# Kernel optimization log

Hardware: AMD Instinct MI355X
Metric: run time of the kernel (lower is better)

Reference implementation:

```python
import jax, jax.numpy as jnp
import numpy as np
from jax import lax

EPS = 1e-6

def setup_inputs() -> dict:
    key = jax.random.key(0)
    ks = jax.random.split(key, 5)
    B, C, H, W = 32, 128, 128, 128
    D = 128
    bcff = jax.random.normal(ks[0], (B, C, H, W), dtype=jnp.float32)
    cur_active = jax.random.randint(ks[1], (B, 1, H, W), 0, 2) > 0
    gamma = jnp.ones((C,), dtype=jnp.float32)
    beta = jnp.zeros((C,), dtype=jnp.float32)
    # trunc_normal_(std=0.02) approximated by clipped normal
    mask_token = jnp.clip(0.02 * jax.random.normal(ks[2], (1, C, 1, 1), dtype=jnp.float32), -0.02, 0.02)
    fan_in = C * 1 * 1
    bound = 1.0 / np.sqrt(fan_in)
    conv_w = jax.random.uniform(ks[3], (D, C, 1, 1), dtype=jnp.float32, minval=-bound, maxval=bound)
    conv_b = jnp.zeros((D,), dtype=jnp.float32)
    return {"bcff": bcff, "cur_active": cur_active, "gamma": gamma, "beta": beta,
            "mask_token": mask_token, "conv_w": conv_w, "conv_b": conv_b}

def reference(bcff, cur_active, gamma, beta, mask_token, conv_w, conv_b):
    # Sparse channels-first LayerNorm: normalize over C at every position; positions
    # that are inactive are overwritten by mask_token (torch zero-fills then where-selects,
    # so the math is identical).
    mu = jnp.mean(bcff, axis=1, keepdims=True)                      # (B,1,H,W)
    var = jnp.mean(jnp.square(bcff - mu), axis=1, keepdims=True)    # biased var, as F.layer_norm
    normed = (bcff - mu) * lax.rsqrt(var + EPS)
    normed = normed * gamma[None, :, None, None] + beta[None, :, None, None]
    # mask-token fill
    filled = jnp.where(cur_active, normed, mask_token)              # (B,C,H,W)
    # 1x1 conv projection (SAME padding, stride 1)
    out = lax.conv_general_dilated(filled, conv_w, window_strides=(1, 1), padding='SAME',
                                   dimension_numbers=('NCHW', 'OIHW', 'NCHW'))
    return out + conv_b[None, :, None, None]
```

## Files before the change

### kernel.cpp

```cpp
#include <hip/hip_runtime.h>


#define CC   128
#define DD   128
#define HWW  16384
#define PP   128
#define NTHREADS 512

typedef __attribute__((ext_vector_type(8))) short short8;
typedef __attribute__((ext_vector_type(4))) float f32x4;

__device__ __forceinline__ float b2f(unsigned short u) {
    return __uint_as_float(((unsigned int)u) << 16);
}
__device__ __forceinline__ unsigned short f2b(float f) {
    unsigned int u = __float_as_uint(f);
    return (unsigned short)((u + 0x7FFFu + ((u >> 16) & 1u)) >> 16);
}
__device__ __forceinline__ unsigned int pk2(float lo, float hi) {
    return (unsigned int)f2b(lo) | ((unsigned int)f2b(hi) << 16);
}
__device__ __forceinline__ float ldf(const void* p, int i, bool bf) {
    return bf ? b2f(((const unsigned short*)p)[i]) : ((const float*)p)[i];
}

__global__ void prep_pack_w(const void* __restrict__ w, unsigned short* __restrict__ wpack,
                            const void* __restrict__ gamma) {
    const bool bf = (((const unsigned int*)gamma)[0] == 0x3F803F80u);
    int e = blockIdx.x * blockDim.x + threadIdx.x;
    int j = e & 7, lane = (e >> 3) & 63, kk = (e >> 9) & 3, wv = e >> 11;
    int d = wv * 16 + (lane & 15);
    int c = kk * 32 + ((lane >> 4) & 3) * 8 + j;
    wpack[e] = f2b(ldf(w, d * CC + c, bf));
}

__global__ __launch_bounds__(NTHREADS, 4)
void spark_densify_mfma(const void* __restrict__ x,
                        const void* __restrict__ act,
                        const void* __restrict__ gam,
                        const void* __restrict__ bet,
                        const void* __restrict__ mtok,
                        const unsigned short* __restrict__ wpack,
                        const void* __restrict__ bias,
                        float* __restrict__ out)
{
    __shared__ __align__(16) uint4 afrag[8 * 4 * 64];
    __shared__ float ps_s[8][PP];
    __shared__ float ps_q[8][PP];
    __shared__ float st_mu[PP];
    __shared__ float st_rs[PP];

    const int t    = threadIdx.x;
    const int bk   = blockIdx.x;
    const int b    = bk >> 7;
    const int pos0 = (bk & 127) * PP;

    const bool bf = (((const unsigned int*)gam)[0] == 0x3F803F80u);
    bool mint = true;
    #pragma unroll
    for (int i = 0; i < 16; ++i) mint = mint && (((const unsigned int*)act)[i] <= 1u);

    const int pq = t & 31;
    const int cg = t >> 5;
    const long xbase = (long)b * CC * HWW + pos0 + pq * 4;

    float4 v[8];
    float s0=0.f,s1=0.f,s2=0.f,s3=0.f;
    float q0=0.f,q1=0.f,q2=0.f,q3=0.f;
    if (!bf) {
        const float* xf = (const float*)x;
        #pragma unroll
        for (int i = 0; i < 8; ++i) {
            v[i] = *(const float4*)(xf + xbase + (long)(cg * 8 + i) * HWW);
            s0 += v[i].x; q0 = fmaf(v[i].x, v[i].x, q0);
            s1 += v[i].y; q1 = fmaf(v[i].y, v[i].y, q1);
            s2 += v[i].z; q2 = fmaf(v[i].z, v[i].z, q2);
            s3 += v[i].w; q3 = fmaf(v[i].w, v[i].w, q3);
        }
    } else {
        const unsigned short* xh = (const unsigned short*)x;
        #pragma unroll
        for (int i = 0; i < 8; ++i) {
            const ushort4 u = *(const ushort4*)(xh + xbase + (long)(cg * 8 + i) * HWW);
            v[i] = make_float4(b2f(u.x), b2f(u.y), b2f(u.z), b2f(u.w));
            s0 += v[i].x; q0 = fmaf(v[i].x, v[i].x, q0);
            s1 += v[i].y; q1 = fmaf(v[i].y, v[i].y, q1);
            s2 += v[i].z; q2 = fmaf(v[i].z, v[i].z, q2);
            s3 += v[i].w; q3 = fmaf(v[i].w, v[i].w, q3);
        }
    }
    s0 += __shfl_xor(s0, 32); q0 += __shfl_xor(q0, 32);
    s1 += __shfl_xor(s1, 32); q1 += __shfl_xor(q1, 32);
    s2 += __shfl_xor(s2, 32); q2 += __shfl_xor(q2, 32);
    s3 += __shfl_xor(s3, 32); q3 += __shfl_xor(q3, 32);

    const int wv_  = t >> 6;
    const int lane = t & 63;
    if (lane < 32) {
        *(float4*)&ps_s[wv_][lane * 4] = make_float4(s0, s1, s2, s3);
        *(float4*)&ps_q[wv_][lane * 4] = make_float4(q0, q1, q2, q3);
    }
    __syncthreads();

    if (t < PP) {
        float ss = 0.f, qq = 0.f;
        #pragma unroll
        for (int w8 = 0; w8 < 8; ++w8) { ss += ps_s[w8][t]; qq += ps_q[w8][t]; }
        const float mu  = ss * (1.0f / 128.0f);
        const float var = qq * (1.0f / 128.0f) - mu * mu;
        st_mu[t] = mu;
        st_rs[t] = rsqrtf(var + 1e-6f);
    }
    __syncthreads();

    {
        const long aoff = (long)b * HWW + pos0 + pq * 4;
        uchar4 a4;
        if (mint) {
            const int4 m = *(const int4*)((const int*)act + aoff);
            a4.x = (unsigned char)(m.x != 0); a4.y = (unsigned char)(m.y != 0);
            a4.z = (unsigned char)(m.z != 0); a4.w = (unsigned char)(m.w != 0);
        } else {
            a4 = *(const uchar4*)((const unsigned char*)act + aoff);
        }
        const float4 muv = *(const float4*)&st_mu[pq * 4];
        const float4 rsv = *(const float4*)&st_rs[pq * 4];
        #pragma unroll
        for (int i = 0; i < 8; ++i) {
            const int c = cg * 8 + i;
            const float gg = ldf(gam,  c, bf);
            const float bb = ldf(bet,  c, bf);
            const float mt = ldf(mtok, c, bf);
            float4 w = v[i];
            w.x = a4.x ? fmaf((w.x - muv.x) * rsv.x, gg, bb) : mt;
            w.y = a4.y ? fmaf((w.y - muv.y) * rsv.y, gg, bb) : mt;
            w.z = a4.z ? fmaf((w.z - muv.z) * rsv.z, gg, bb) : mt;
            w.w = a4.w ? fmaf((w.w - muv.w) * rsv.w, gg, bb) : mt;
            v[i] = w;
        }
    }

    {
        const int kk = cg >> 2;
        const int sb = 16 * (cg & 3);
        #pragma unroll
        for (int k = 0; k < 4; ++k) {
            const int p    = pq * 4 + k;
            const int pt   = p >> 4;
            const int slot = (p & 15) + sb;
            const int idx  = (pt * 4 + kk) * 64 + (slot ^ pt);
            uint4 wq;
            if      (k == 0) wq = make_uint4(pk2(v[0].x,v[1].x), pk2(v[2].x,v[3].x),
                                             pk2(v[4].x,v[5].x), pk2(v[6].x,v[7].x));
            else if (k == 1) wq = make_uint4(pk2(v[0].y,v[1].y), pk2(v[2].y,v[3].y),
                                             pk2(v[4].y,v[5].y), pk2(v[6].y,v[7].y));
            else if (k == 2) wq = make_uint4(pk2(v[0].z,v[1].z), pk2(v[2].z,v[3].z),
                                             pk2(v[4].z,v[5].z), pk2(v[6].z,v[7].z));
            else             wq = make_uint4(pk2(v[0].w,v[1].w), pk2(v[2].w,v[3].w),
                                             pk2(v[4].w,v[5].w), pk2(v[6].w,v[7].w));
            afrag[idx] = wq;
        }
    }
    __syncthreads();

    const int wv = __builtin_amdgcn_readfirstlane(t >> 6);

    short8 bw[4];
    #pragma unroll
    for (int kk = 0; kk < 4; ++kk)
        bw[kk] = *(const short8*)(wpack + ((wv * 4 + kk) * 64 + lane) * 8);

    f32x4 acc[8];
    #pragma unroll
    for (int pt = 0; pt < 8; ++pt) acc[pt] = (f32x4){0.f, 0.f, 0.f, 0.f};

    #pragma unroll
    for (int pt = 0; pt < 8; ++pt) {
        #pragma unroll
        for (int kk = 0; kk < 4; ++kk) {
            const short8 a = *(const short8*)&afrag[(pt * 4 + kk) * 64 + (lane ^ pt)];
            acc[pt] = __builtin_amdgcn_mfma_f32_16x16x32_bf16(a, bw[kk], acc[pt], 0, 0, 0);
        }
    }

    const int   dch   = wv * 16 + (lane & 15);
    const float bb    = ldf(bias, dch, bf);
    const long  obase = (long)b * DD * HWW + (long)dch * HWW + pos0 + (lane >> 4) * 4;
    #pragma unroll
    for (int pt = 0; pt < 8; ++pt) {
        float4 o;
        o.x = acc[pt][0] + bb; o.y = acc[pt][1] + bb;
        o.z = acc[pt][2] + bb; o.w = acc[pt][3] + bb;
        *(float4*)(out + obase + pt * 16) = o;
    }
}

extern "C" void kernel_launch(void* const* d_in, const int* in_sizes, int n_in,
                              void* d_out, int out_size, void* d_ws, size_t ws_size,
                              hipStream_t stream) {
    const void* x     = d_in[0];
    const void* act   = d_in[1];
    const void* gamma = d_in[2];
    const void* beta  = d_in[3];
    const void* mtok  = d_in[4];
    const void* convw = d_in[5];
    const void* bias  = d_in[6];
    float* out = (float*)d_out;
    unsigned short* wpack = (unsigned short*)d_ws;

    prep_pack_w<<<64, 256, 0, stream>>>(convw, wpack, gamma);

    const int nblocks = (32 * HWW) / PP;
    spark_densify_mfma<<<nblocks, NTHREADS, 0, stream>>>(
        x, act, gamma, beta, mtok, wpack, bias, out);
}
```

Measured before the change: 452.2 us.

## Fold LayerNorm and mask-token into GEMM epilogue, feed raw activations to MFMA

Rewrites the math so raw x (cast to bf16) goes straight into the MFMA. Gamma is folded into the packed weights, and per-position rsqrt, mean and active flag plus per-channel precomputed vectors (g1, cm, dd) are applied in the epilogue. This takes the normalisation and select pass off the critical path between the stats reduction and the GEMM, removing one barrier stage. Blocks shrink to 64 positions with 256 threads and each wave computes two 16-channel output tiles. Quantising raw x to bf16 instead of normalised values, and the cancellation in the epilogue form, may cost accuracy when the mean is large.

```diff
diff --git a/kernel.cpp b/kernel.cpp
--- a/kernel.cpp
+++ b/kernel.cpp
@@ -1,11 +1,12 @@
 #include <hip/hip_runtime.h>
+#include <hip/hip_bf16.h>
 
 
 #define CC   128
 #define DD   128
 #define HWW  16384
-#define PP   128
-#define NTHREADS 512
+#define PP   64
+#define TPB  256
 
 typedef __attribute__((ext_vector_type(8))) short short8;
 typedef __attribute__((ext_vector_type(4))) float f32x4;
@@ -24,44 +25,72 @@
     return bf ? b2f(((const unsigned short*)p)[i]) : ((const float*)p)[i];
 }
 
-__global__ void prep_pack_w(const void* __restrict__ w, unsigned short* __restrict__ wpack,
-                            const void* __restrict__ gamma) {
+__global__ void prep_pack_w(const void* __restrict__ w, const void* __restrict__ gamma,
+                            unsigned short* __restrict__ wpack) {
     const bool bf = (((const unsigned int*)gamma)[0] == 0x3F803F80u);
     int e = blockIdx.x * blockDim.x + threadIdx.x;
-    int j = e & 7, lane = (e >> 3) & 63, kk = (e >> 9) & 3, wv = e >> 11;
-    int d = wv * 16 + (lane & 15);
+    int j = e & 7, lane = (e >> 3) & 63, kk = (e >> 9) & 3, g = e >> 11;
+    int d = g * 16 + (lane & 15);
     int c = kk * 32 + ((lane >> 4) & 3) * 8 + j;
-    wpack[e] = f2b(ldf(w, d * CC + c, bf));
-}
-
-__global__ __launch_bounds__(NTHREADS, 4)
-void spark_densify_mfma(const void* __restrict__ x,
-                        const void* __restrict__ act,
-                        const void* __restrict__ gam,
-                        const void* __restrict__ bet,
-                        const void* __restrict__ mtok,
-                        const unsigned short* __restrict__ wpack,
-                        const void* __restrict__ bias,
-                        float* __restrict__ out)
+    wpack[e] = f2b(ldf(w, d * CC + c, bf) * ldf(gamma, c, bf));
+}
+
+__global__ void prep_vec(const void* __restrict__ w, const void* __restrict__ gamma,
+                         const void* __restrict__ beta, const void* __restrict__ mtok,
+                         const void* __restrict__ bias, float* __restrict__ g1b,
+                         float* __restrict__ cmb, float* __restrict__ ddb) {
+    const bool bf = (((const unsigned int*)gamma)[0] == 0x3F803F80u);
+    const int d = threadIdx.x;
+    float g1 = 0.f, cm = 0.f, dd = 0.f;
+    for (int c = 0; c < CC; ++c) {
+        const float wv = ldf(w, d * CC + c, bf);
+        g1 += b2f(f2b(wv * ldf(gamma, c, bf)));
+        cm = fmaf(wv, ldf(mtok, c, bf), cm);
+        dd = fmaf(wv, ldf(beta, c, bf) - ldf(mtok, c, bf), dd);
+    }
+    g1b[d] = g1;
+    cmb[d] = cm + ldf(bias, d, bf);
+    ddb[d] = dd;
+}
+
+__global__ __launch_bounds__(TPB, 4)
+void spark_densify_v6(const void* __restrict__ x,
+                      const void* __restrict__ act,
+                      const void* __restrict__ gam,
+                      const unsigned short* __restrict__ wpack,
+                      const float* __restrict__ g1b,
+                      const float* __restrict__ cmb,
+                      const float* __restrict__ ddb,
+                      float* __restrict__ out)
 {
-    __shared__ __align__(16) uint4 afrag[8 * 4 * 64];
-    __shared__ float ps_s[8][PP];
-    __shared__ float ps_q[8][PP];
-    __shared__ float st_mu[PP];
-    __shared__ float st_rs[PP];
+    __shared__ __align__(16) uint4 afrag[16 * 64];
+    __shared__ __align__(16) float ps_s[4][PP];
+    __shared__ __align__(16) float ps_q[4][PP];
+    __shared__ __align__(16) float st_rsa[PP];
+    __shared__ __align__(16) float st_t1[PP];
+    __shared__ __align__(16) float st_a[PP];
 
     const int t    = threadIdx.x;
+    const int wv   = t >> 6;
+    const int lane = t & 63;
     const int bk   = blockIdx.x;
-    const int b    = bk >> 7;
-    const int pos0 = (bk & 127) * PP;
+    const int b    = bk >> 8;
+    const int pos0 = (bk & 255) * PP;
 
     const bool bf = (((const unsigned int*)gam)[0] == 0x3F803F80u);
     bool mint = true;
     #pragma unroll
     for (int i = 0; i < 16; ++i) mint = mint && (((const unsigned int*)act)[i] <= 1u);
 
-    const int pq = t & 31;
-    const int cg = t >> 5;
+    short8 bw[2][4];
+    #pragma unroll
+    for (int dt = 0; dt < 2; ++dt)
+        #pragma unroll
+        for (int kk = 0; kk < 4; ++kk)
+            bw[dt][kk] = *(const short8*)(wpack + (((wv * 2 + dt) * 4 + kk) * 64 + lane) * 8);
+
+    const int pq = t & 15;
+    const int cg = t >> 4;
     const long xbase = (long)b * CC * HWW + pos0 + pq * 4;
 
     float4 v[8];
@@ -89,55 +118,17 @@
             s3 += v[i].w; q3 = fmaf(v[i].w, v[i].w, q3);
         }
     }
+    s0 += __shfl_xor(s0, 16); q0 += __shfl_xor(q0, 16);
+    s1 += __shfl_xor(s1, 16); q1 += __shfl_xor(q1, 16);
+    s2 += __shfl_xor(s2, 16); q2 += __shfl_xor(q2, 16);
+    s3 += __shfl_xor(s3, 16); q3 += __shfl_xor(q3, 16);
     s0 += __shfl_xor(s0, 32); q0 += __shfl_xor(q0, 32);
     s1 += __shfl_xor(s1, 32); q1 += __shfl_xor(q1, 32);
     s2 += __shfl_xor(s2, 32); q2 += __shfl_xor(q2, 32);
     s3 += __shfl_xor(s3, 32); q3 += __shfl_xor(q3, 32);
-
-    const int wv_  = t >> 6;
-    const int lane = t & 63;
-    if (lane < 32) {
-        *(float4*)&ps_s[wv_][lane * 4] = make_float4(s0, s1, s2, s3);
-        *(float4*)&ps_q[wv_][lane * 4] = make_float4(q0, q1, q2, q3);
-    }
-    __syncthreads();
-
-    if (t < PP) {
-        float ss = 0.f, qq = 0.f;
-        #pragma unroll
-        for (int w8 = 0; w8 < 8; ++w8) { ss += ps_s[w8][t]; qq += ps_q[w8][t]; }
-        const float mu  = ss * (1.0f / 128.0f);
-        const float var = qq * (1.0f / 128.0f) - mu * mu;
-        st_mu[t] = mu;
-        st_rs[t] = rsqrtf(var + 1e-6f);
-    }
-    __syncthreads();
-
-    {
-        const long aoff = (long)b * HWW + pos0 + pq * 4;
-        uchar4 a4;
-        if (mint) {
-            const int4 m = *(const int4*)((const int*)act + aoff);
-            a4.x = (unsigned char)(m.x != 0); a4.y = (unsigned char)(m.y != 0);
-            a4.z = (unsigned char)(m.z != 0); a4.w = (unsigned char)(m.w != 0);
-        } else {
-            a4 = *(const uchar4*)((const unsigned char*)act + aoff);
-        }
-        const float4 muv = *(const float4*)&st_mu[pq * 4];
-        const float4 rsv = *(const float4*)&st_rs[pq * 4];
-        #pragma unroll
-        for (int i = 0; i < 8; ++i) {
-            const int c = cg * 8 + i;
-            const float gg = ldf(gam,  c, bf);
-            const float bb = ldf(bet,  c, bf);
-            const float mt = ldf(mtok, c, bf);
-            float4 w = v[i];
-            w.x = a4.x ? fmaf((w.x - muv.x) * rsv.x, gg, bb) : mt;
-            w.y = a4.y ? fmaf((w.y - muv.y) * rsv.y, gg, bb) : mt;
-            w.z = a4.z ? fmaf((w.z - muv.z) * rsv.z, gg, bb) : mt;
-            w.w = a4.w ? fmaf((w.w - muv.w) * rsv.w, gg, bb) : mt;
-            v[i] = w;
-        }
+    if (lane < 16) {
+        *(float4*)&ps_s[wv][lane * 4] = make_float4(s0, s1, s2, s3);
+        *(float4*)&ps_q[wv][lane * 4] = make_float4(q0, q1, q2, q3);
     }
 
     {
@@ -145,9 +136,8 @@
         const int sb = 16 * (cg & 3);
         #pragma unroll
         for (int k = 0; k < 4; ++k) {
-            const int p    = pq * 4 + k;
-            const int pt   = p >> 4;
-            const int slot = (p & 15) + sb;
+            const int pt   = pq >> 2;
+            const int slot = (pq & 3) * 4 + k + sb;
             const int idx  = (pt * 4 + kk) * 64 + (slot ^ pt);
             uint4 wq;
             if      (k == 0) wq = make_uint4(pk2(v[0].x,v[1].x), pk2(v[2].x,v[3].x),
@@ -155,43 +145,70 @@
             else if (k == 1) wq = make_uint4(pk2(v[0].y,v[1].y), pk2(v[2].y,v[3].y),
                                              pk2(v[4].y,v[5].y), pk2(v[6].y,v[7].y));
             else if (k == 2) wq = make_uint4(pk2(v[0].z,v[1].z), pk2(v[2].z,v[3].z),
-                                             pk2(v[4].z,v[5].z), pk2(v[6].z,v[7].z));
+                                             pk2(v[4].z,v[5].z), pk2(v[6].z,v[5].z));
             else             wq = make_uint4(pk2(v[0].w,v[1].w), pk2(v[2].w,v[3].w),
                                              pk2(v[4].w,v[5].w), pk2(v[6].w,v[7].w));
+            if (k == 2) wq = make_uint4(pk2(v[0].z,v[1].z), pk2(v[2].z,v[3].z),
+                                        pk2(v[4].z,v[5].z), pk2(v[6].z,v[7].z));
             afrag[idx] = wq;
         }
     }
     __syncthreads();
 
-    const int wv = __builtin_amdgcn_readfirstlane(t >> 6);
-
-    short8 bw[4];
-    #pragma unroll
-    for (int kk = 0; kk < 4; ++kk)
-        bw[kk] = *(const short8*)(wpack + ((wv * 4 + kk) * 64 + lane) * 8);
-
-    f32x4 acc[8];
-    #pragma unroll
-    for (int pt = 0; pt < 8; ++pt) acc[pt] = (f32x4){0.f, 0.f, 0.f, 0.f};
-
-    #pragma unroll
-    for (int pt = 0; pt < 8; ++pt) {
-        #pragma unroll
-        for (int kk = 0; kk < 4; ++kk) {
-            const short8 a = *(const short8*)&afrag[(pt * 4 + kk) * 64 + (lane ^ pt)];
-            acc[pt] = __builtin_amdgcn_mfma_f32_16x16x32_bf16(a, bw[kk], acc[pt], 0, 0, 0);
-        }
-    }
-
-    const int   dch   = wv * 16 + (lane & 15);
-    const float bb    = ldf(bias, dch, bf);
-    const long  obase = (long)b * DD * HWW + (long)dch * HWW + pos0 + (lane >> 4) * 4;
-    #pragma unroll
-    for (int pt = 0; pt < 8; ++pt) {
-        float4 o;
-        o.x = acc[pt][0] + bb; o.y = acc[pt][1] + bb;
-        o.z = acc[pt][2] + bb; o.w = acc[pt][3] + bb;
-        *(float4*)(out + obase + pt * 16) = o;
+    if (t < PP) {
+        float ss = ps_s[0][t] + ps_s[1][t] + ps_s[2][t] + ps_s[3][t];
+        float qq = ps_q[0][t] + ps_q[1][t] + ps_q[2][t] + ps_q[3][t];
+        const float mu  = ss * (1.0f / 128.0f);
+        const float var = qq * (1.0f / 128.0f) - mu * mu;
+        const float rs  = rsqrtf(var + 1e-6f);
+        const long  ap  = (long)b * HWW + pos0 + t;
+        const bool  a   = mint ? (((const int*)act)[ap] != 0)
+                               : (((const unsigned char*)act)[ap] != 0);
+        const float af  = a ? 1.f : 0.f;
+        st_rsa[t] = af * rs;
+        st_t1[t]  = -af * rs * mu;
+        st_a[t]   = af;
+    }
+
+    f32x4 acc[2][4];
+    #pragma unroll
+    for (int dt = 0; dt < 2; ++dt)
+        #pragma unroll
+        for (int pt = 0; pt < 4; ++pt) acc[dt][pt] = (f32x4){0.f, 0.f, 0.f, 0.f};
+
+    #pragma unroll
+    for (int pt = 0; pt < 4; ++pt) {
+        short8 af_[4];
+        #pragma unroll
+        for (int kk = 0; kk < 4; ++kk)
+            af_[kk] = *(const short8*)&afrag[(pt * 4 + kk) * 64 + (lane ^ pt)];
+        #pragma unroll
+        for (int dt = 0; dt < 2; ++dt)
+            #pragma unroll
+            for (int kk = 0; kk < 4; ++kk)
+                acc[dt][pt] = __builtin_amdgcn_mfma_f32_16x16x32_bf16(
+                                  af_[kk], bw[dt][kk], acc[dt][pt], 0, 0, 0);
+    }
+    __syncthreads();
+
+    const int rg = (lane >> 4) * 4;
+    #pragma unroll
+    for (int pt = 0; pt < 4; ++pt) {
+        const int p0 = pt * 16 + rg;
+        const float4 rsa = *(const float4*)&st_rsa[p0];
+        const float4 t1  = *(const float4*)&st_t1[p0];
+        const float4 av  = *(const float4*)&st_a[p0];
+        #pragma unroll
+        for (int dt = 0; dt < 2; ++dt) {
+            const int dch = wv * 32 + dt * 16 + (lane & 15);
+            const float g1 = g1b[dch], cm = cmb[dch], dd = ddb[dch];
+            float4 o;
+            o.x = fmaf(rsa.x, acc[dt][pt][0], fmaf(t1.x, g1, fmaf(av.x, dd, cm)));
+            o.y = fmaf(rsa.y, acc[dt][pt][1], fmaf(t1.y, g1, fmaf(av.y, dd, cm)));
+            o.z = fmaf(rsa.z, acc[dt][pt][2], fmaf(t1.z, g1, fmaf(av.z, dd, cm)));
+            o.w = fmaf(rsa.w, acc[dt][pt][3], fmaf(t1.w, g1, fmaf(av.w, dd, cm)));
+            *(float4*)(out + (long)b * DD * HWW + (long)dch * HWW + pos0 + p0) = o;
+        }
     }
 }
 
@@ -206,11 +223,16 @@
     const void* convw = d_in[5];
     const void* bias  = d_in[6];
     float* out = (float*)d_out;
+
     unsigned short* wpack = (unsigned short*)d_ws;
-
-    prep_pack_w<<<64, 256, 0, stream>>>(convw, wpack, gamma);
+    float* g1b = (float*)((char*)d_ws + 32768);
+    float* cmb = g1b + DD;
+    float* ddb = cmb + DD;
+
+    prep_pack_w<<<64, 256, 0, stream>>>(convw, gamma, wpack);
+    prep_vec<<<1, DD, 0, stream>>>(convw, gamma, beta, mtok, bias, g1b, cmb, ddb);
 
     const int nblocks = (32 * HWW) / PP;
-    spark_densify_mfma<<<nblocks, NTHREADS, 0, stream>>>(
-        x, act, gamma, beta, mtok, wpack, bias, out);
-}
+    spark_densify_v6<<<nblocks, TPB, 0, stream>>>(
+        x, act, gamma, wpack, g1b, cmb, ddb, out);
+}
```

New measurement: 489.9 us. 8.3% more time.
